# Kernel tuning notes

Measured on AMD Instinct MI355X. Metric: run time of the kernel, lower is better.

The kernel has to match this reference:

```python
import jax, jax.numpy as jnp
import numpy as np

B, S, D = 2048, 200, 128   # batch, n_steps, embedding dim per vector
H = 64                      # hidden_dim
MASK_SCALE = 1e10


def setup_inputs() -> dict:
    key = jax.random.key(0)
    ks = jax.random.split(key, 6)
    his = jax.random.normal(ks[0], (B, S, D), dtype=jnp.float32)
    target = jax.random.normal(ks[1], (B, 1, D), dtype=jnp.float32)
    # mask == 1.0 marks padded history positions (they get -1e10 added pre-softmax)
    mask = (jax.random.uniform(ks[2], (B, S)) < 0.3).astype(jnp.float32)
    W = jax.random.normal(ks[3], (3 * D, H), dtype=jnp.float32) * 0.1
    W_bias = jnp.full((H,), 0.1, dtype=jnp.float32)
    O = jax.random.normal(ks[4], (H, 1), dtype=jnp.float32) * 0.1
    O_bias = jnp.full((1,), 0.1, dtype=jnp.float32)
    return {"his": his, "target": target, "mask": mask,
            "W": W, "W_bias": W_bias, "O": O, "O_bias": O_bias}


def reference(his, target, mask, W, W_bias, O, O_bias):
    tgt = jnp.broadcast_to(target, his.shape)          # [B,S,D] tile over steps
    diff = his - tgt
    att_vec = jnp.concatenate([his, diff, tgt], axis=2)  # [B,S,3D]
    h = jax.nn.relu(jnp.einsum('bsf,fh->bsh', att_vec, W) + W_bias)  # [B,S,H]
    alpha = jnp.einsum('bsh,ho->bso', h, O) + O_bias   # [B,S,1]
    alpha = alpha[:, :, 0] - mask * MASK_SCALE         # [B,S]
    attn = jax.nn.softmax(alpha, axis=-1)              # [B,S]
    out = jnp.einsum('bs,bsd->bd', attn, his)          # weighted-sum pooling
    return out
```

## Files before the change

kernel.cpp:

```cpp
#include <hip/hip_runtime.h>

#define B_ 2048
#define S_ 200
#define D_ 128
#define H_ 64
#define MASK_SCALE 1e10f

typedef __attribute__((ext_vector_type(8))) short short8_t;
typedef __attribute__((ext_vector_type(4))) float f32x4;
typedef __attribute__((ext_vector_type(4))) unsigned short ushort4_t;

__device__ __forceinline__ unsigned short f2bf(float f) {
    unsigned u = __float_as_uint(f);
    unsigned r = (u + 0x7fffu + ((u >> 16) & 1u)) >> 16;
    return (unsigned short)r;
}
__device__ __forceinline__ float bf2f(unsigned short v) {
    return __uint_as_float(((unsigned)v) << 16);
}

__global__ __launch_bounds__(256) void prep(const float* __restrict__ W,
                                            const float* __restrict__ W_bias,
                                            const float* __restrict__ target,
                                            unsigned short* __restrict__ wfrag,
                                            float* __restrict__ tproj) {
    const int blk = blockIdx.x;
    const int t = threadIdx.x;
    if (blk < 32) {
        int idx = blk * 256 + t;
        int d = idx >> 6;
        int h = idx & 63;
        float w1 = W[d * H_ + h];
        float w2 = W[(D_ + d) * H_ + h];
        int kt = d >> 5, q = (d >> 3) & 3, j = d & 7;
        int nt = h >> 4, lm = h & 15;
        int lane = (q << 4) | lm;
        wfrag[((kt * 4 + nt) * 64 + lane) * 8 + j] = f2bf(w1 + w2);
    } else {
        int lane = t & 63, wv = t >> 6;
        int bb = (blk - 32) * 4 + wv;
        const float* tg = target + (size_t)bb * D_;
        float acc = W_bias[lane];
        #pragma unroll 4
        for (int d = 0; d < D_; ++d) {
            float w2 = W[(D_ + d) * H_ + lane];
            float w3 = W[(2 * D_ + d) * H_ + lane];
            acc = fmaf(tg[d], w3 - w2, acc);
        }
        tproj[bb * H_ + lane] = acc;
    }
}

__global__ __launch_bounds__(256, 3) void fused_kernel(const float* __restrict__ his,
                                                       const float* __restrict__ mask,
                                                       const unsigned short* __restrict__ wfrag,
                                                       const float* __restrict__ tproj,
                                                       const float* __restrict__ Ovec,
                                                       float* __restrict__ out) {
    __shared__ unsigned short hisb[S_ * D_];
    __shared__ float alpha_s[208];
    __shared__ float red8[8];
    __shared__ float tp_s[H_];
    __shared__ float ov_s[H_];
    __shared__ float pool_s[3 * D_];

    const int b    = blockIdx.x;
    const int t    = threadIdx.x;
    const int lane = t & 63;
    const int wv   = t >> 6;
    const int lm   = lane & 15;
    const int q    = lane >> 4;

    float mk = (t < S_) ? mask[(size_t)b * S_ + t] : 0.f;
    if (t < H_) {
        tp_s[t] = tproj[b * H_ + t];
        ov_s[t] = Ovec[t];
    }

    short8_t bfrag[16];
    #pragma unroll
    for (int f = 0; f < 16; ++f)
        bfrag[f] = *(const short8_t*)(wfrag + ((size_t)(f * 64 + lane)) * 8);

    const float4* hb4 = (const float4*)(his + (size_t)b * S_ * D_);
    #pragma unroll
    for (int g = 0; g < 5; ++g) {
        float4 x[5];
        #pragma unroll
        for (int j = 0; j < 5; ++j)
            x[j] = hb4[t + (g * 5 + j) * 256];
        #pragma unroll
        for (int j = 0; j < 5; ++j) {
            int i  = t + (g * 5 + j) * 256;
            int s  = i >> 5;
            int d8 = i & 31;
            int pc = (d8 >> 1) ^ (s & 15);
            ushort4_t v;
            v[0] = f2bf(x[j].x); v[1] = f2bf(x[j].y);
            v[2] = f2bf(x[j].z); v[3] = f2bf(x[j].w);
            *(ushort4_t*)((char*)hisb + s * 256 + pc * 16 + (d8 & 1) * 8) = v;
        }
    }
    __syncthreads();

    for (int tile = wv; tile < 13; tile += 4) {
        int row0 = tile * 16;
        int ar = row0 + lm; if (ar > S_ - 1) ar = S_ - 1;

        f32x4 acc[4];
        #pragma unroll
        for (int nt = 0; nt < 4; ++nt) acc[nt] = (f32x4){0.f, 0.f, 0.f, 0.f};

        #pragma unroll
        for (int kt = 0; kt < 4; ++kt) {
            int c = (kt * 4 + q) ^ (ar & 15);
            short8_t a = *(const short8_t*)((const char*)hisb + ar * 256 + c * 16);
            #pragma unroll
            for (int nt = 0; nt < 4; ++nt)
                acc[nt] = __builtin_amdgcn_mfma_f32_16x16x32_bf16(a, bfrag[kt * 4 + nt], acc[nt], 0, 0, 0);
        }

        float part[4];
        #pragma unroll
        for (int r = 0; r < 4; ++r) {
            float sum = 0.f;
            #pragma unroll
            for (int nt = 0; nt < 4; ++nt) {
                int h = nt * 16 + lm;
                float v = acc[nt][r] + tp_s[h];
                v = fmaxf(v, 0.f);
                sum = fmaf(v, ov_s[h], sum);
            }
            part[r] = sum;
        }
        #pragma unroll
        for (int off = 1; off < 16; off <<= 1) {
            #pragma unroll
            for (int r = 0; r < 4; ++r)
                part[r] += __shfl_xor(part[r], off);
        }
        if (lm == 0) {
            #pragma unroll
            for (int r = 0; r < 4; ++r)
                alpha_s[row0 + q * 4 + r] = part[r];
        }
    }
    __syncthreads();

    float a = (t < S_) ? alpha_s[t] - mk * MASK_SCALE : -INFINITY;
    float m = a;
    #pragma unroll
    for (int off = 1; off < 64; off <<= 1) m = fmaxf(m, __shfl_xor(m, off));
    if (lane == 0) red8[wv] = m;
    __syncthreads();
    m = fmaxf(fmaxf(red8[0], red8[1]), fmaxf(red8[2], red8[3]));
    float e = (t < S_) ? __expf(a - m) : 0.f;
    float ssum = e;
    #pragma unroll
    for (int off = 1; off < 64; off <<= 1) ssum += __shfl_xor(ssum, off);
    if (lane == 0) red8[4 + wv] = ssum;
    __syncthreads();
    float inv = 1.f / (red8[4] + red8[5] + red8[6] + red8[7]);
    __syncthreads();
    if (t < S_) alpha_s[t] = e * inv;
    __syncthreads();

    const int d8 = t & 31;
    const int sg = t >> 5;
    float acc0 = 0.f, acc1 = 0.f, acc2 = 0.f, acc3 = 0.f;
    #pragma unroll 5
    for (int s = sg; s < S_; s += 8) {
        float w = alpha_s[s];
        int pc = (d8 >> 1) ^ (s & 15);
        ushort4_t v = *(const ushort4_t*)((const char*)hisb + s * 256 + pc * 16 + (d8 & 1) * 8);
        acc0 = fmaf(w, bf2f(v[0]), acc0);
        acc1 = fmaf(w, bf2f(v[1]), acc1);
        acc2 = fmaf(w, bf2f(v[2]), acc2);
        acc3 = fmaf(w, bf2f(v[3]), acc3);
    }
    acc0 += __shfl_xor(acc0, 32);
    acc1 += __shfl_xor(acc1, 32);
    acc2 += __shfl_xor(acc2, 32);
    acc3 += __shfl_xor(acc3, 32);
    if (wv && lane < 32) {
        float4 p; p.x = acc0; p.y = acc1; p.z = acc2; p.w = acc3;
        *(float4*)(&pool_s[(wv - 1) * D_ + d8 * 4]) = p;
    }
    __syncthreads();
    if (wv == 0 && lane < 32) {
        #pragma unroll
        for (int k = 0; k < 3; ++k) {
            const float4 p = *(const float4*)(&pool_s[k * D_ + d8 * 4]);
            acc0 += p.x; acc1 += p.y; acc2 += p.z; acc3 += p.w;
        }
        float4 o; o.x = acc0; o.y = acc1; o.z = acc2; o.w = acc3;
        *(float4*)(out + (size_t)b * D_ + d8 * 4) = o;
    }
}

extern "C" void kernel_launch(void* const* d_in, const int* in_sizes, int n_in,
                              void* d_out, int out_size, void* d_ws, size_t ws_size,
                              hipStream_t stream) {
    const float* his    = (const float*)d_in[0];
    const float* target = (const float*)d_in[1];
    const float* mask   = (const float*)d_in[2];
    const float* W      = (const float*)d_in[3];
    const float* W_bias = (const float*)d_in[4];
    const float* Ovec   = (const float*)d_in[5];
    float* out = (float*)d_out;

    char* ws = (char*)d_ws;
    unsigned short* wfrag = (unsigned short*)ws;
    float* tproj          = (float*)(ws + 16384);

    prep<<<544, 256, 0, stream>>>(W, W_bias, target, wfrag, tproj);
    fused_kernel<<<B_, 256, 0, stream>>>(his, mask, wfrag, tproj, Ovec, out);
}
```

Baseline: 320.1 us.

## Split fused attention kernel into row-parallel alpha kernel and pooling kernel

Replaces the single per-batch fused kernel with two kernels. The first computes attention logits over flattened rows with MFMA, loading his directly from global memory into registers with no LDS staging. The second does masked softmax and fp32 weighted pooling, reading his from global again. This removes the 51KB LDS buffer and its occupancy limit, at the cost of reading his from HBM twice (about 210MB each pass) plus an extra launch and a round trip for alpha.

```diff
diff --git a/kernel.cpp b/kernel.cpp
--- a/kernel.cpp
+++ b/kernel.cpp
@@ -4,19 +4,16 @@
 #define S_ 200
 #define D_ 128
 #define H_ 64
+#define ROWS (B_ * S_)
 #define MASK_SCALE 1e10f
 
 typedef __attribute__((ext_vector_type(8))) short short8_t;
 typedef __attribute__((ext_vector_type(4))) float f32x4;
-typedef __attribute__((ext_vector_type(4))) unsigned short ushort4_t;
 
 __device__ __forceinline__ unsigned short f2bf(float f) {
     unsigned u = __float_as_uint(f);
     unsigned r = (u + 0x7fffu + ((u >> 16) & 1u)) >> 16;
     return (unsigned short)r;
-}
-__device__ __forceinline__ float bf2f(unsigned short v) {
-    return __uint_as_float(((unsigned)v) << 16);
 }
 
 __global__ __launch_bounds__(256) void prep(const float* __restrict__ W,
@@ -51,103 +48,92 @@
     }
 }
 
-__global__ __launch_bounds__(256, 3) void fused_kernel(const float* __restrict__ his,
-                                                       const float* __restrict__ mask,
-                                                       const unsigned short* __restrict__ wfrag,
-                                                       const float* __restrict__ tproj,
-                                                       const float* __restrict__ Ovec,
-                                                       float* __restrict__ out) {
-    __shared__ unsigned short hisb[S_ * D_];
-    __shared__ float alpha_s[208];
+__global__ __launch_bounds__(256) void alpha_kernel(const float* __restrict__ his,
+                                                    const unsigned short* __restrict__ wfrag,
+                                                    const float* __restrict__ tproj,
+                                                    const float* __restrict__ Ovec,
+                                                    float* __restrict__ alpha) {
+    const int lane = threadIdx.x & 63;
+    const int wv = threadIdx.x >> 6;
+    const int tile = blockIdx.x * 4 + wv;
+    const int row0 = tile * 16;
+    const int lm = lane & 15;
+    const int q = lane >> 4;
+
+    const float* hp = his + (size_t)(row0 + lm) * D_ + q * 8;
+    float4 x[8];
+    #pragma unroll
+    for (int kt = 0; kt < 4; ++kt) {
+        x[2 * kt]     = *(const float4*)(hp + kt * 32);
+        x[2 * kt + 1] = *(const float4*)(hp + kt * 32 + 4);
+    }
+
+    short8_t bfrag[16];
+    #pragma unroll
+    for (int f = 0; f < 16; ++f)
+        bfrag[f] = *(const short8_t*)(wfrag + ((size_t)(f * 64 + lane)) * 8);
+
+    f32x4 acc[4];
+    #pragma unroll
+    for (int nt = 0; nt < 4; ++nt) acc[nt] = (f32x4){0.f, 0.f, 0.f, 0.f};
+
+    #pragma unroll
+    for (int kt = 0; kt < 4; ++kt) {
+        short8_t a;
+        a[0] = f2bf(x[2*kt].x); a[1] = f2bf(x[2*kt].y);
+        a[2] = f2bf(x[2*kt].z); a[3] = f2bf(x[2*kt].w);
+        a[4] = f2bf(x[2*kt+1].x); a[5] = f2bf(x[2*kt+1].y);
+        a[6] = f2bf(x[2*kt+1].z); a[7] = f2bf(x[2*kt+1].w);
+        #pragma unroll
+        for (int nt = 0; nt < 4; ++nt)
+            acc[nt] = __builtin_amdgcn_mfma_f32_16x16x32_bf16(a, bfrag[kt * 4 + nt], acc[nt], 0, 0, 0);
+    }
+
+    float part[4];
+    #pragma unroll
+    for (int r = 0; r < 4; ++r) {
+        int grow = row0 + q * 4 + r;
+        int b = grow / S_;
+        const float* tp = tproj + b * H_;
+        float sum = 0.f;
+        #pragma unroll
+        for (int nt = 0; nt < 4; ++nt) {
+            int h = nt * 16 + lm;
+            float v = acc[nt][r] + tp[h];
+            v = fmaxf(v, 0.f);
+            sum = fmaf(v, Ovec[h], sum);
+        }
+        part[r] = sum;
+    }
+    #pragma unroll
+    for (int off = 1; off < 16; off <<= 1) {
+        #pragma unroll
+        for (int r = 0; r < 4; ++r)
+            part[r] += __shfl_xor(part[r], off);
+    }
+    if (lm == 0) {
+        #pragma unroll
+        for (int r = 0; r < 4; ++r)
+            alpha[row0 + q * 4 + r] = part[r];
+    }
+}
+
+__global__ __launch_bounds__(256) void pool_kernel(const float* __restrict__ his,
+                                                   const float* __restrict__ alpha,
+                                                   const float* __restrict__ mask,
+                                                   float* __restrict__ out) {
+    __shared__ float wgt[S_];
     __shared__ float red8[8];
-    __shared__ float tp_s[H_];
-    __shared__ float ov_s[H_];
     __shared__ float pool_s[3 * D_];
 
     const int b    = blockIdx.x;
     const int t    = threadIdx.x;
     const int lane = t & 63;
     const int wv   = t >> 6;
-    const int lm   = lane & 15;
-    const int q    = lane >> 4;
-
-    float mk = (t < S_) ? mask[(size_t)b * S_ + t] : 0.f;
-    if (t < H_) {
-        tp_s[t] = tproj[b * H_ + t];
-        ov_s[t] = Ovec[t];
-    }
-
-    short8_t bfrag[16];
-    #pragma unroll
-    for (int f = 0; f < 16; ++f)
-        bfrag[f] = *(const short8_t*)(wfrag + ((size_t)(f * 64 + lane)) * 8);
-
-    const float4* hb4 = (const float4*)(his + (size_t)b * S_ * D_);
-    #pragma unroll
-    for (int g = 0; g < 5; ++g) {
-        float4 x[5];
-        #pragma unroll
-        for (int j = 0; j < 5; ++j)
-            x[j] = hb4[t + (g * 5 + j) * 256];
-        #pragma unroll
-        for (int j = 0; j < 5; ++j) {
-            int i  = t + (g * 5 + j) * 256;
-            int s  = i >> 5;
-            int d8 = i & 31;
-            int pc = (d8 >> 1) ^ (s & 15);
-            ushort4_t v;
-            v[0] = f2bf(x[j].x); v[1] = f2bf(x[j].y);
-            v[2] = f2bf(x[j].z); v[3] = f2bf(x[j].w);
-            *(ushort4_t*)((char*)hisb + s * 256 + pc * 16 + (d8 & 1) * 8) = v;
-        }
-    }
-    __syncthreads();
-
-    for (int tile = wv; tile < 13; tile += 4) {
-        int row0 = tile * 16;
-        int ar = row0 + lm; if (ar > S_ - 1) ar = S_ - 1;
-
-        f32x4 acc[4];
-        #pragma unroll
-        for (int nt = 0; nt < 4; ++nt) acc[nt] = (f32x4){0.f, 0.f, 0.f, 0.f};
-
-        #pragma unroll
-        for (int kt = 0; kt < 4; ++kt) {
-            int c = (kt * 4 + q) ^ (ar & 15);
-            short8_t a = *(const short8_t*)((const char*)hisb + ar * 256 + c * 16);
-            #pragma unroll
-            for (int nt = 0; nt < 4; ++nt)
-                acc[nt] = __builtin_amdgcn_mfma_f32_16x16x32_bf16(a, bfrag[kt * 4 + nt], acc[nt], 0, 0, 0);
-        }
-
-        float part[4];
-        #pragma unroll
-        for (int r = 0; r < 4; ++r) {
-            float sum = 0.f;
-            #pragma unroll
-            for (int nt = 0; nt < 4; ++nt) {
-                int h = nt * 16 + lm;
-                float v = acc[nt][r] + tp_s[h];
-                v = fmaxf(v, 0.f);
-                sum = fmaf(v, ov_s[h], sum);
-            }
-            part[r] = sum;
-        }
-        #pragma unroll
-        for (int off = 1; off < 16; off <<= 1) {
-            #pragma unroll
-            for (int r = 0; r < 4; ++r)
-                part[r] += __shfl_xor(part[r], off);
-        }
-        if (lm == 0) {
-            #pragma unroll
-            for (int r = 0; r < 4; ++r)
-                alpha_s[row0 + q * 4 + r] = part[r];
-        }
-    }
-    __syncthreads();
-
-    float a = (t < S_) ? alpha_s[t] - mk * MASK_SCALE : -INFINITY;
+
+    float a = -INFINITY;
+    if (t < S_)
+        a = alpha[(size_t)b * S_ + t] - mask[(size_t)b * S_ + t] * MASK_SCALE;
     float m = a;
     #pragma unroll
     for (int off = 1; off < 64; off <<= 1) m = fmaxf(m, __shfl_xor(m, off));
@@ -161,22 +147,21 @@
     if (lane == 0) red8[4 + wv] = ssum;
     __syncthreads();
     float inv = 1.f / (red8[4] + red8[5] + red8[6] + red8[7]);
-    __syncthreads();
-    if (t < S_) alpha_s[t] = e * inv;
-    __syncthreads();
-
-    const int d8 = t & 31;
+    if (t < S_) wgt[t] = e * inv;
+    __syncthreads();
+
+    const int d4 = t & 31;
     const int sg = t >> 5;
+    const float4* hb4 = (const float4*)(his + (size_t)b * S_ * D_);
     float acc0 = 0.f, acc1 = 0.f, acc2 = 0.f, acc3 = 0.f;
     #pragma unroll 5
     for (int s = sg; s < S_; s += 8) {
-        float w = alpha_s[s];
-        int pc = (d8 >> 1) ^ (s & 15);
-        ushort4_t v = *(const ushort4_t*)((const char*)hisb + s * 256 + pc * 16 + (d8 & 1) * 8);
-        acc0 = fmaf(w, bf2f(v[0]), acc0);
-        acc1 = fmaf(w, bf2f(v[1]), acc1);
-        acc2 = fmaf(w, bf2f(v[2]), acc2);
-        acc3 = fmaf(w, bf2f(v[3]), acc3);
+        float w = wgt[s];
+        float4 v = hb4[s * 32 + d4];
+        acc0 = fmaf(w, v.x, acc0);
+        acc1 = fmaf(w, v.y, acc1);
+        acc2 = fmaf(w, v.z, acc2);
+        acc3 = fmaf(w, v.w, acc3);
     }
     acc0 += __shfl_xor(acc0, 32);
     acc1 += __shfl_xor(acc1, 32);
@@ -184,17 +169,17 @@
     acc3 += __shfl_xor(acc3, 32);
     if (wv && lane < 32) {
         float4 p; p.x = acc0; p.y = acc1; p.z = acc2; p.w = acc3;
-        *(float4*)(&pool_s[(wv - 1) * D_ + d8 * 4]) = p;
+        *(float4*)(&pool_s[(wv - 1) * D_ + d4 * 4]) = p;
     }
     __syncthreads();
     if (wv == 0 && lane < 32) {
         #pragma unroll
         for (int k = 0; k < 3; ++k) {
-            const float4 p = *(const float4*)(&pool_s[k * D_ + d8 * 4]);
+            const float4 p = *(const float4*)(&pool_s[k * D_ + d4 * 4]);
             acc0 += p.x; acc1 += p.y; acc2 += p.z; acc3 += p.w;
         }
         float4 o; o.x = acc0; o.y = acc1; o.z = acc2; o.w = acc3;
-        *(float4*)(out + (size_t)b * D_ + d8 * 4) = o;
+        *(float4*)(out + (size_t)b * D_ + d4 * 4) = o;
     }
 }
 
@@ -212,7 +197,9 @@
     char* ws = (char*)d_ws;
     unsigned short* wfrag = (unsigned short*)ws;
     float* tproj          = (float*)(ws + 16384);
+    float* alpha          = (float*)(ws + 16384 + 524288);
 
     prep<<<544, 256, 0, stream>>>(W, W_bias, target, wfrag, tproj);
-    fused_kernel<<<B_, 256, 0, stream>>>(his, mask, wfrag, tproj, Ovec, out);
-}
+    alpha_kernel<<<ROWS / 64, 256, 0, stream>>>(his, wfrag, tproj, Ovec, alpha);
+    pool_kernel<<<B_, 256, 0, stream>>>(his, alpha, mask, out);
+}
```

New measurement: 339.6 us. 1.06x slower.
